# Optimization experiments

Hardware: AMD Instinct MI355X
Metric: run time of the kernel (lower is better)

## Reference

```python
import jax, jax.numpy as jnp
import numpy as np

B, T, L, D, H = 8, 8192, 256, 512, 8
HD = D // H  # head_dim = 64


def setup_inputs() -> dict:
    key = jax.random.key(0)
    ks = jax.random.split(key, 6)
    s = 0.02
    return {
        "x": jax.random.normal(ks[0], (B, T, D), jnp.float32),
        "query": jax.random.normal(ks[1], (B, L, D), jnp.float32),
        "Wq": jax.random.normal(ks[2], (D, D), jnp.float32) * s,
        "bq": jnp.zeros((D,), jnp.float32),
        "Wkv": jax.random.normal(ks[3], (D, 2 * D), jnp.float32) * s,
        "bkv": jnp.zeros((2 * D,), jnp.float32),
        "Wproj": jax.random.normal(ks[4], (D, D), jnp.float32) * s,
        "bproj": jnp.zeros((D,), jnp.float32),
    }


def reference(x, query, Wq, bq, Wkv, bkv, Wproj, bproj):
    scale = HD ** (-0.5)
    # projections (weights stored [in, out]; equivalent to torch Linear with W.T)
    q = (query @ Wq + bq).reshape(B, L, H, HD).transpose(0, 2, 1, 3)   # [B,H,L,hd]
    kv = (x @ Wkv + bkv).reshape(B, T, 2, H, HD)
    k = kv[:, :, 0].transpose(0, 2, 1, 3)                              # [B,H,T,hd]
    v = kv[:, :, 1].transpose(0, 2, 1, 3)                              # [B,H,T,hd]
    # scaled dot-product attention, full L x T scores as in original
    attn = jnp.einsum("bhld,bhtd->bhlt", q * scale, k)                 # [B,H,L,T]
    attn = jax.nn.softmax(attn, axis=-1)
    out = jnp.einsum("bhlt,bhtd->bhld", attn, v)                       # [B,H,L,hd]
    out = out.transpose(0, 2, 1, 3).reshape(B, L, D)
    return out @ Wproj + bproj
```

## Files before the change

kernel.cpp:

```cpp
#include <hip/hip_runtime.h>
#include <hip/hip_bf16.h>
#include <cstdint>
#include <cstddef>

typedef __bf16 bf16_t;
typedef __bf16 bf16x8 __attribute__((ext_vector_type(8)));
typedef __bf16 bf16x4 __attribute__((ext_vector_type(4)));
typedef float  f32x4  __attribute__((ext_vector_type(4)));

#define DEVI __device__ __forceinline__

constexpr int B_ = 8, T_ = 8192, L_ = 256, D_ = 512, H_ = 8, HD_ = 64;
constexpr float SCALE_LOG2E = 0.125f * 1.44269504088896340736f;
constexpr int NSPLIT = 8;

DEVI float fast_exp2(float x) {
#if __has_builtin(__builtin_amdgcn_exp2f)
  return __builtin_amdgcn_exp2f(x);
#else
  return exp2f(x);
#endif
}

DEVI void async16(void* lds_base, const void* gptr, int lane) {
#if __has_builtin(__builtin_amdgcn_global_load_lds)
  __builtin_amdgcn_global_load_lds(
      (__attribute__((address_space(1))) void*)gptr,
      (__attribute__((address_space(3))) void*)lds_base, 16, 0, 0);
  (void)lane;
#else
  ((bf16x8*)lds_base)[lane] = *(const bf16x8*)gptr;
#endif
}

__global__ __launch_bounds__(256) void cvt_f32_to_bf16(
    const float* __restrict__ in, bf16_t* __restrict__ out, int n4) {
  int stride = gridDim.x * blockDim.x;
  for (int i = blockIdx.x * blockDim.x + threadIdx.x; i < n4; i += stride) {
    float4 v = ((const float4*)in)[i];
    bf16x4 o;
    o[0] = (bf16_t)v.x; o[1] = (bf16_t)v.y; o[2] = (bf16_t)v.z; o[3] = (bf16_t)v.w;
    ((bf16x4*)out)[i] = o;
  }
}

__global__ __launch_bounds__(256) void transpose_cvt(
    const float* __restrict__ W, bf16_t* __restrict__ WT, int K, int N, float scale) {
  __shared__ float tile[32][33];
  const int tx = threadIdx.x & 31, ty = threadIdx.x >> 5;
  const int n0 = blockIdx.x * 32, k0 = blockIdx.y * 32;
#pragma unroll
  for (int i = 0; i < 4; ++i)
    tile[ty + i * 8][tx] = W[(size_t)(k0 + ty + i * 8) * N + n0 + tx];
  __syncthreads();
#pragma unroll
  for (int i = 0; i < 4; ++i)
    WT[(size_t)(n0 + ty + i * 8) * K + k0 + tx] = (bf16_t)(tile[tx][ty + i * 8] * scale);
}

template <int MODE>
__global__ __launch_bounds__(256, 4) void gemm_bf16(
    const bf16_t* __restrict__ A, const bf16_t* __restrict__ BT,
    const float* __restrict__ bias, float bscale,
    bf16_t* __restrict__ out0, bf16_t* __restrict__ out1,
    float* __restrict__ outf) {
  constexpr int K = 512;
  __shared__ __align__(16) union SM {
    bf16_t stage[2][128 * 64];
    bf16_t cs[128 * 136];
  } sm;

  const int tid = threadIdx.x;
  const int w = tid >> 6, lane = tid & 63;
  const int m0 = blockIdx.x * 128, n0 = blockIdx.y * 128;
  const int wm = w & 1, wn = w >> 1;

  f32x4 acc[4][4] = {};

  const int sw = ((lane & 7) ^ ((lane >> 3) & 7)) * 8;
  const bf16_t* aG = A + (size_t)(m0 + w * 32 + (lane >> 3)) * K + sw;
  const bf16_t* bG = BT + (size_t)(n0 + w * 32 + (lane >> 3)) * K + sw;
  bf16_t* aL = &sm.stage[0][(w * 32) * 64];
  bf16_t* bL = &sm.stage[1][(w * 32) * 64];

  for (int k0 = 0; k0 < K; k0 += 64) {
#pragma unroll
    for (int i = 0; i < 4; ++i) {
      async16(aL + i * (8 * 64), aG + k0 + (size_t)(i * 8) * K, lane);
      async16(bL + i * (8 * 64), bG + k0 + (size_t)(i * 8) * K, lane);
    }
    __syncthreads();
#pragma unroll
    for (int kk = 0; kk < 2; ++kk) {
      bf16x8 af[4], bfr[4];
      const int cc = ((kk * 4 + (lane >> 4)) ^ (lane & 7)) * 8;
#pragma unroll
      for (int mt = 0; mt < 4; ++mt)
        af[mt] = *(const bf16x8*)&sm.stage[0][(wm * 64 + mt * 16 + (lane & 15)) * 64 + cc];
#pragma unroll
      for (int nt = 0; nt < 4; ++nt)
        bfr[nt] = *(const bf16x8*)&sm.stage[1][(wn * 64 + nt * 16 + (lane & 15)) * 64 + cc];
#pragma unroll
      for (int mt = 0; mt < 4; ++mt)
#pragma unroll
        for (int nt = 0; nt < 4; ++nt)
          acc[mt][nt] = __builtin_amdgcn_mfma_f32_16x16x32_bf16(af[mt], bfr[nt], acc[mt][nt], 0, 0, 0);
    }
    __syncthreads();
  }

  if (MODE == 2) {
#pragma unroll
    for (int nt = 0; nt < 4; ++nt) {
      const int col = n0 + wn * 64 + nt * 16 + (lane & 15);
      const float bv = bias[col];
#pragma unroll
      for (int mt = 0; mt < 4; ++mt)
#pragma unroll
        for (int r = 0; r < 4; ++r) {
          const int row = m0 + wm * 64 + mt * 16 + (lane >> 4) * 4 + r;
          outf[(size_t)row * D_ + col] = acc[mt][nt][r] + bv;
        }
    }
    return;
  }

  const bool vside = (MODE == 1) && (n0 >= 512);

#pragma unroll
  for (int nt = 0; nt < 4; ++nt) {
    const int col = wn * 64 + nt * 16 + (lane & 15);
    const float bv = bias[n0 + col] * bscale;
#pragma unroll
    for (int mt = 0; mt < 4; ++mt)
#pragma unroll
      for (int r = 0; r < 4; ++r) {
        const int row = wm * 64 + mt * 16 + (lane >> 4) * 4 + r;
        if (vside) sm.cs[col * 136 + row] = (bf16_t)(acc[mt][nt][r] + bv);
        else       sm.cs[row * 136 + col] = (bf16_t)(acc[mt][nt][r] + bv);
      }
  }
  __syncthreads();

  if (MODE == 0) {
#pragma unroll
    for (int i = 0; i < 8; ++i) {
      const int c = tid + i * 256;
      const int row = c >> 4, col = (c & 15) * 8;
      const int gr = m0 + row;
      const int b = gr >> 8, l = gr & 255;
      const int h = (n0 + col) >> 6, hd = (n0 + col) & 63;
      *(float4*)&out0[((size_t)(b * 8 + h) * L_ + l) * 64 + hd] =
          *(const float4*)&sm.cs[row * 136 + col];
    }
  } else if (!vside) {
#pragma unroll
    for (int i = 0; i < 8; ++i) {
      const int c = tid + i * 256;
      const int row = c >> 4, col = (c & 15) * 8;
      const int gr = m0 + row;
      const int b = gr >> 13, t = gr & 8191;
      const int h = (n0 + col) >> 6, hd = (n0 + col) & 63;
      *(float4*)&out0[((size_t)(b * 8 + h) * T_ + t) * 64 + hd] =
          *(const float4*)&sm.cs[row * 136 + col];
    }
  } else {
    const int b = m0 >> 13, t0 = m0 & 8191;
#pragma unroll
    for (int i = 0; i < 8; ++i) {
      const int c = tid + i * 256;
      const int tc = c & 15, ch = c >> 4;
      const int h = (n0 - 512 + ch) >> 6, hd = ch & 63;
      *(float4*)&out1[((size_t)(b * 8 + h) * 64 + hd) * T_ + t0 + tc * 8] =
          *(const float4*)&sm.cs[ch * 136 + tc * 8];
    }
  }
}

__global__ __launch_bounds__(256, 4) void attn_fwd(
    const bf16_t* __restrict__ qg, const bf16_t* __restrict__ kg,
    const bf16_t* __restrict__ vg, float* __restrict__ Opart,
    float* __restrict__ lbuf) {
  __shared__ __align__(16) bf16_t KPs[10240];
  __shared__ __align__(16) bf16_t Vs[4 * 64 * 32];
  bf16_t* Ks = KPs;
  bf16_t* Ps = KPs;
  bf16_t* Qs = KPs;

  const int n = blockIdx.x;
  const int split = n & 7, qt = (n >> 3) & 3, bh = n >> 5;
  const int tid = threadIdx.x;
  const int w = tid >> 6, lane = tid & 63;

  {
    const bf16_t* src = qg + ((size_t)bh * L_ + qt * 64) * 64;
    const int row = w * 16 + (lane >> 2);
#pragma unroll
    for (int hh = 0; hh < 2; ++hh)
      async16(&Qs[hh * 2048 + (w * 16) * 32],
              src + (size_t)row * 64 + hh * 32 + (lane & 3) * 8, lane);
  }
  __syncthreads();

  bf16x8 aq[2];
#pragma unroll
  for (int hh = 0; hh < 2; ++hh)
    aq[hh] = *(const bf16x8*)&Qs[hh * 2048 + (w * 16 + (lane & 15)) * 32 + (lane >> 4) * 8];
  __syncthreads();

  bf16x8 ones;
#pragma unroll
  for (int j = 0; j < 8; ++j) ones[j] = (bf16_t)1.0f;

  f32x4 O[4] = {};
  f32x4 lacc = {0.f, 0.f, 0.f, 0.f};

  const int kt0 = split * (T_ / 128 / NSPLIT);
  for (int kt = kt0; kt < kt0 + T_ / 128 / NSPLIT; ++kt) {
#pragma unroll
    for (int hh = 0; hh < 2; ++hh)
#pragma unroll
      for (int i = 0; i < 2; ++i) {
        const int trow = kt * 128 + w * 32 + i * 16 + (lane >> 2);
        async16(&Ks[hh * 4096 + (w * 32 + i * 16) * 32],
                kg + ((size_t)bh * T_ + trow) * 64 + hh * 32 + (lane & 3) * 8, lane);
      }
#pragma unroll
    for (int kc = 0; kc < 4; ++kc) {
      const int hd = w * 16 + (lane >> 2);
      async16(&Vs[kc * 2048 + (w * 16) * 32],
              vg + ((size_t)bh * 64 + hd) * T_ + kt * 128 + kc * 32 + (lane & 3) * 8, lane);
    }
    __syncthreads();

    f32x4 S[8];
#pragma unroll
    for (int nt = 0; nt < 8; ++nt) {
      bf16x8 b0 = *(const bf16x8*)&Ks[0 * 4096 + (nt * 16 + (lane & 15)) * 32 + (lane >> 4) * 8];
      bf16x8 b1 = *(const bf16x8*)&Ks[1 * 4096 + (nt * 16 + (lane & 15)) * 32 + (lane >> 4) * 8];
      f32x4 s = {0.f, 0.f, 0.f, 0.f};
      s = __builtin_amdgcn_mfma_f32_16x16x32_bf16(aq[0], b0, s, 0, 0, 0);
      s = __builtin_amdgcn_mfma_f32_16x16x32_bf16(aq[1], b1, s, 0, 0, 0);
#pragma unroll
      for (int r = 0; r < 4; ++r) s[r] = fast_exp2(s[r]);
      S[nt] = s;
    }

    __syncthreads();

#pragma unroll
    for (int nt = 0; nt < 8; ++nt)
#pragma unroll
      for (int r = 0; r < 4; ++r) {
        const int rp = w * 16 + (lane >> 4) * 4 + r;
        Ps[(nt >> 1) * 2560 + rp * 40 + (nt & 1) * 16 + (lane & 15)] = (bf16_t)S[nt][r];
      }

    __syncthreads();

#pragma unroll
    for (int kc = 0; kc < 4; ++kc) {
      bf16x8 ap = *(const bf16x8*)&Ps[kc * 2560 + (w * 16 + (lane & 15)) * 40 + (lane >> 4) * 8];
      lacc = __builtin_amdgcn_mfma_f32_16x16x32_bf16(ap, ones, lacc, 0, 0, 0);
#pragma unroll
      for (int n2 = 0; n2 < 4; ++n2) {
        bf16x8 bv = *(const bf16x8*)&Vs[kc * 2048 + (n2 * 16 + (lane & 15)) * 32 + (lane >> 4) * 8];
        O[n2] = __builtin_amdgcn_mfma_f32_16x16x32_bf16(ap, bv, O[n2], 0, 0, 0);
      }
    }
    __syncthreads();
  }

  const int part = ((bh * 4 + qt) * NSPLIT + split);
  float* op = Opart + (size_t)part * 64 * 64;
#pragma unroll
  for (int n2 = 0; n2 < 4; ++n2) {
#pragma unroll
    for (int r = 0; r < 4; ++r) {
      const int row = w * 16 + (lane >> 4) * 4 + r;
      op[(size_t)row * 64 + n2 * 16 + (lane & 15)] = O[n2][r];
    }
  }
  if ((lane & 15) == 0) {
    float* lb = lbuf + (size_t)part * 64;
#pragma unroll
    for (int r = 0; r < 4; ++r)
      lb[w * 16 + (lane >> 4) * 4 + r] = lacc[r];
  }
}

__global__ __launch_bounds__(256) void attn_combine(
    const float* __restrict__ Opart, const float* __restrict__ lbuf,
    bf16_t* __restrict__ og) {
  const int blk = blockIdx.x;
  const int bh = blk >> 2, qt = blk & 3;
  const int tid = threadIdx.x;
  const int row = tid >> 2, c0 = (tid & 3) * 16;
  float L = 0.f;
#pragma unroll
  for (int s = 0; s < NSPLIT; ++s) L += lbuf[((size_t)blk * NSPLIT + s) * 64 + row];
  const float inv = 1.f / L;
  f32x4 acc[4] = {};
  const float* ob = Opart + (size_t)blk * NSPLIT * 4096 + row * 64 + c0;
#pragma unroll
  for (int s = 0; s < NSPLIT; ++s)
#pragma unroll
    for (int j = 0; j < 4; ++j) {
      f32x4 v = *(const f32x4*)&ob[s * 4096 + j * 4];
      acc[j] += v;
    }
  const int b = bh >> 3, h = bh & 7;
  bf16_t* dst = og + ((size_t)(b * L_ + qt * 64 + row)) * D_ + h * 64 + c0;
#pragma unroll
  for (int j = 0; j < 4; ++j) {
    bf16x4 o;
#pragma unroll
    for (int e = 0; e < 4; ++e) o[e] = (bf16_t)(acc[j][e] * inv);
    *(bf16x4*)&dst[j * 4] = o;
  }
}

extern "C" void kernel_launch(void* const* d_in, const int* in_sizes, int n_in,
                              void* d_out, int out_size, void* d_ws, size_t ws_size,
                              hipStream_t stream) {
  const float* x     = (const float*)d_in[0];
  const float* query = (const float*)d_in[1];
  const float* Wq    = (const float*)d_in[2];
  const float* bq    = (const float*)d_in[3];
  const float* Wkv   = (const float*)d_in[4];
  const float* bkv   = (const float*)d_in[5];
  const float* Wproj = (const float*)d_in[6];
  const float* bproj = (const float*)d_in[7];
  float* out = (float*)d_out;

  char* ws = (char*)d_ws;
  bf16_t* xb   = (bf16_t*)(ws + 0);
  float*  Opart = (float*)(ws + 0);
  float*  lbuf  = (float*)(ws + 34603008);
  bf16_t* wkvT = (bf16_t*)(ws + 67108864);
  bf16_t* wqT  = (bf16_t*)(ws + 68157440);
  bf16_t* qin  = (bf16_t*)(ws + 68681728);
  bf16_t* qh   = (bf16_t*)(ws + 70778880);
  bf16_t* kh   = (bf16_t*)(ws + 72876032);
  bf16_t* vTh  = (bf16_t*)(ws + 139984896);
  bf16_t* attnb = (bf16_t*)(ws + 207093760);
  bf16_t* wprojT = (bf16_t*)(ws + 209190912);

  cvt_f32_to_bf16<<<4096, 256, 0, stream>>>(x, xb, (B_ * T_ * D_) / 4);
  cvt_f32_to_bf16<<<1024, 256, 0, stream>>>(query, qin, (B_ * L_ * D_) / 4);
  transpose_cvt<<<dim3(16, 16), 256, 0, stream>>>(Wq, wqT, 512, 512, SCALE_LOG2E);
  transpose_cvt<<<dim3(32, 16), 256, 0, stream>>>(Wkv, wkvT, 512, 1024, 1.0f);
  transpose_cvt<<<dim3(16, 16), 256, 0, stream>>>(Wproj, wprojT, 512, 512, 1.0f);
  gemm_bf16<0><<<dim3(16, 4), 256, 0, stream>>>(qin, wqT, bq, SCALE_LOG2E, qh, nullptr, nullptr);
  gemm_bf16<1><<<dim3(512, 8), 256, 0, stream>>>(xb, wkvT, bkv, 1.0f, kh, vTh, nullptr);
  attn_fwd<<<dim3(64 * 4 * NSPLIT), 256, 0, stream>>>(qh, kh, vTh, Opart, lbuf);
  attn_combine<<<dim3(256), 256, 0, stream>>>(Opart, lbuf, attnb);
  gemm_bf16<2><<<dim3(16, 4), 256, 0, stream>>>(attnb, wprojT, bproj, 1.0f, nullptr, nullptr, out);
}
```

Before: 419.0 us.

## Add dedicated 256x256-tile KV projection GEMM with XCD-aware block mapping

```diff
diff --git a/kernel.cpp b/kernel.cpp
--- a/kernel.cpp
+++ b/kernel.cpp
@@ -62,7 +62,7 @@
 __global__ __launch_bounds__(256, 4) void gemm_bf16(
     const bf16_t* __restrict__ A, const bf16_t* __restrict__ BT,
     const float* __restrict__ bias, float bscale,
-    bf16_t* __restrict__ out0, bf16_t* __restrict__ out1,
+    bf16_t* __restrict__ out0,
     float* __restrict__ outf) {
   constexpr int K = 512;
   __shared__ __align__(16) union SM {
@@ -125,8 +125,6 @@
     return;
   }
 
-  const bool vside = (MODE == 1) && (n0 >= 512);
-
 #pragma unroll
   for (int nt = 0; nt < 4; ++nt) {
     const int col = wn * 64 + nt * 16 + (lane & 15);
@@ -136,43 +134,157 @@
 #pragma unroll
       for (int r = 0; r < 4; ++r) {
         const int row = wm * 64 + mt * 16 + (lane >> 4) * 4 + r;
-        if (vside) sm.cs[col * 136 + row] = (bf16_t)(acc[mt][nt][r] + bv);
-        else       sm.cs[row * 136 + col] = (bf16_t)(acc[mt][nt][r] + bv);
+        sm.cs[row * 136 + col] = (bf16_t)(acc[mt][nt][r] + bv);
       }
   }
   __syncthreads();
 
-  if (MODE == 0) {
-#pragma unroll
-    for (int i = 0; i < 8; ++i) {
-      const int c = tid + i * 256;
-      const int row = c >> 4, col = (c & 15) * 8;
-      const int gr = m0 + row;
-      const int b = gr >> 8, l = gr & 255;
-      const int h = (n0 + col) >> 6, hd = (n0 + col) & 63;
-      *(float4*)&out0[((size_t)(b * 8 + h) * L_ + l) * 64 + hd] =
-          *(const float4*)&sm.cs[row * 136 + col];
-    }
-  } else if (!vside) {
-#pragma unroll
-    for (int i = 0; i < 8; ++i) {
-      const int c = tid + i * 256;
-      const int row = c >> 4, col = (c & 15) * 8;
-      const int gr = m0 + row;
-      const int b = gr >> 13, t = gr & 8191;
-      const int h = (n0 + col) >> 6, hd = (n0 + col) & 63;
-      *(float4*)&out0[((size_t)(b * 8 + h) * T_ + t) * 64 + hd] =
-          *(const float4*)&sm.cs[row * 136 + col];
+#pragma unroll
+  for (int i = 0; i < 8; ++i) {
+    const int c = tid + i * 256;
+    const int row = c >> 4, col = (c & 15) * 8;
+    const int gr = m0 + row;
+    const int b = gr >> 8, l = gr & 255;
+    const int h = (n0 + col) >> 6, hd = (n0 + col) & 63;
+    *(float4*)&out0[((size_t)(b * 8 + h) * L_ + l) * 64 + hd] =
+        *(const float4*)&sm.cs[row * 136 + col];
+  }
+}
+
+__global__ __launch_bounds__(512, 2) void gemm_kv(
+    const bf16_t* __restrict__ A, const bf16_t* __restrict__ BT,
+    const float* __restrict__ bias,
+    bf16_t* __restrict__ kh, bf16_t* __restrict__ vTh) {
+  constexpr int K = 512;
+  __shared__ __align__(16) union SM {
+    bf16_t stage[2][2][256 * 64];
+    bf16_t cs[128 * 264];
+  } sm;
+
+  const int tid = threadIdx.x;
+  const int w = tid >> 6, lane = tid & 63;
+  const int wm = w & 1, wn = w >> 1;
+
+  const int b = blockIdx.x;
+  const int xcd = b & 7, idx = b >> 3;
+  const int m0 = ((xcd << 5) | (idx >> 2)) * 256;
+  const int n0 = (idx & 3) * 256;
+
+  f32x4 acc[8][4] = {};
+
+  const int sw = ((lane & 7) ^ ((lane >> 3) & 7)) * 8;
+  const int rl = w * 8 + (lane >> 3);
+
+  {
+    bf16_t* As = sm.stage[0][0];
+    bf16_t* Bs = sm.stage[0][1];
+#pragma unroll
+    for (int i = 0; i < 4; ++i)
+      async16(As + (i * 64 + w * 8) * 64, A + (size_t)(m0 + i * 64 + rl) * K + sw, lane);
+#pragma unroll
+    for (int i = 0; i < 4; ++i)
+      async16(Bs + (i * 64 + w * 8) * 64, BT + (size_t)(n0 + i * 64 + rl) * K + sw, lane);
+  }
+
+  for (int t = 0; t < 8; ++t) {
+    __syncthreads();
+    if (t < 7) {
+      bf16_t* As = sm.stage[(t + 1) & 1][0];
+      bf16_t* Bs = sm.stage[(t + 1) & 1][1];
+      const int k0 = (t + 1) * 64;
+#pragma unroll
+      for (int i = 0; i < 4; ++i)
+        async16(As + (i * 64 + w * 8) * 64, A + (size_t)(m0 + i * 64 + rl) * K + k0 + sw, lane);
+#pragma unroll
+      for (int i = 0; i < 4; ++i)
+        async16(Bs + (i * 64 + w * 8) * 64, BT + (size_t)(n0 + i * 64 + rl) * K + k0 + sw, lane);
+    }
+    const bf16_t* As = sm.stage[t & 1][0];
+    const bf16_t* Bs = sm.stage[t & 1][1];
+#pragma unroll
+    for (int kk = 0; kk < 2; ++kk) {
+      const int cc = ((kk * 4 + (lane >> 4)) ^ (lane & 7)) * 8;
+      bf16x8 bfr[4];
+#pragma unroll
+      for (int nt = 0; nt < 4; ++nt)
+        bfr[nt] = *(const bf16x8*)&Bs[(wn * 64 + nt * 16 + (lane & 15)) * 64 + cc];
+#pragma unroll
+      for (int mh = 0; mh < 2; ++mh) {
+        bf16x8 af[4];
+#pragma unroll
+        for (int mt = 0; mt < 4; ++mt)
+          af[mt] = *(const bf16x8*)&As[(wm * 128 + (mh * 4 + mt) * 16 + (lane & 15)) * 64 + cc];
+#pragma unroll
+        for (int mt = 0; mt < 4; ++mt)
+#pragma unroll
+          for (int nt = 0; nt < 4; ++nt)
+            acc[mh * 4 + mt][nt] = __builtin_amdgcn_mfma_f32_16x16x32_bf16(
+                af[mt], bfr[nt], acc[mh * 4 + mt][nt], 0, 0, 0);
+      }
+    }
+  }
+  __syncthreads();
+
+  float bv[4];
+#pragma unroll
+  for (int nt = 0; nt < 4; ++nt)
+    bv[nt] = bias[n0 + wn * 64 + nt * 16 + (lane & 15)];
+
+  if (n0 < 512) {
+#pragma unroll
+    for (int mh = 0; mh < 2; ++mh) {
+      if (wm == mh) {
+#pragma unroll
+        for (int a = 0; a < 8; ++a)
+#pragma unroll
+          for (int nt = 0; nt < 4; ++nt)
+#pragma unroll
+            for (int r = 0; r < 4; ++r) {
+              const int rowL = a * 16 + (lane >> 4) * 4 + r;
+              const int col = wn * 64 + nt * 16 + (lane & 15);
+              sm.cs[rowL * 264 + col] = (bf16_t)(acc[a][nt][r] + bv[nt]);
+            }
+      }
+      __syncthreads();
+#pragma unroll
+      for (int i = 0; i < 8; ++i) {
+        const int c = tid + i * 512;
+        const int row = c >> 5, col = (c & 31) * 8;
+        const int gr = m0 + mh * 128 + row;
+        const int bb = gr >> 13, tt = gr & 8191;
+        const int h = (n0 + col) >> 6, hd = (n0 + col) & 63;
+        *(float4*)&kh[((size_t)(bb * 8 + h) * T_ + tt) * 64 + hd] =
+            *(const float4*)&sm.cs[row * 264 + col];
+      }
+      __syncthreads();
     }
   } else {
-    const int b = m0 >> 13, t0 = m0 & 8191;
-#pragma unroll
-    for (int i = 0; i < 8; ++i) {
-      const int c = tid + i * 256;
-      const int tc = c & 15, ch = c >> 4;
-      const int h = (n0 - 512 + ch) >> 6, hd = ch & 63;
-      *(float4*)&out1[((size_t)(b * 8 + h) * 64 + hd) * T_ + t0 + tc * 8] =
-          *(const float4*)&sm.cs[ch * 136 + tc * 8];
+    const int bb = m0 >> 13, t0 = m0 & 8191;
+#pragma unroll
+    for (int nh = 0; nh < 2; ++nh) {
+      if ((wn >> 1) == nh) {
+#pragma unroll
+        for (int a = 0; a < 8; ++a)
+#pragma unroll
+          for (int nt = 0; nt < 4; ++nt)
+#pragma unroll
+            for (int r = 0; r < 4; ++r) {
+              const int row = wm * 128 + a * 16 + (lane >> 4) * 4 + r;
+              const int colL = (wn & 1) * 64 + nt * 16 + (lane & 15);
+              sm.cs[colL * 264 + row] = (bf16_t)(acc[a][nt][r] + bv[nt]);
+            }
+      }
+      __syncthreads();
+#pragma unroll
+      for (int i = 0; i < 8; ++i) {
+        const int c = tid + i * 512;
+        const int colL = c >> 5, tb = (c & 31) * 8;
+        const int ch = (n0 - 512) + nh * 128 + colL;
+        const int h = ch >> 6, hd = ch & 63;
+        *(float4*)&vTh[((size_t)(bb * 8 + h) * 64 + hd) * T_ + t0 + tb] =
+            *(const float4*)&sm.cs[colL * 264 + tb];
+      }
+      __syncthreads();
     }
   }
 }
@@ -351,9 +463,9 @@
   transpose_cvt<<<dim3(16, 16), 256, 0, stream>>>(Wq, wqT, 512, 512, SCALE_LOG2E);
   transpose_cvt<<<dim3(32, 16), 256, 0, stream>>>(Wkv, wkvT, 512, 1024, 1.0f);
   transpose_cvt<<<dim3(16, 16), 256, 0, stream>>>(Wproj, wprojT, 512, 512, 1.0f);
-  gemm_bf16<0><<<dim3(16, 4), 256, 0, stream>>>(qin, wqT, bq, SCALE_LOG2E, qh, nullptr, nullptr);
-  gemm_bf16<1><<<dim3(512, 8), 256, 0, stream>>>(xb, wkvT, bkv, 1.0f, kh, vTh, nullptr);
+  gemm_bf16<0><<<dim3(16, 4), 256, 0, stream>>>(qin, wqT, bq, SCALE_LOG2E, qh, nullptr);
+  gemm_kv<<<dim3(1024), 512, 0, stream>>>(xb, wkvT, bkv, kh, vTh);
   attn_fwd<<<dim3(64 * 4 * NSPLIT), 256, 0, stream>>>(qh, kh, vTh, Opart, lbuf);
   attn_combine<<<dim3(256), 256, 0, stream>>>(Opart, lbuf, attnb);
-  gemm_bf16<2><<<dim3(16, 4), 256, 0, stream>>>(attnb, wprojT, bproj, 1.0f, nullptr, nullptr, out);
-}
+  gemm_bf16<2><<<dim3(16, 4), 256, 0, stream>>>(attnb, wprojT, bproj, 1.0f, nullptr, out);
+}
```

After: 395.4 us. 5.6% less time.
